# Kernel optimization log

Hardware: AMD Instinct MI355X
Metric: run time of the kernel (lower is better)

## Reference

```python
import jax, jax.numpy as jnp
import numpy as np

B, T, DIM = 2, 2048, 2048
N_HEADS, N_KV_HEADS = 16, 4
HEAD_DIM = DIM // N_HEADS  # 128
N_REP = N_HEADS // N_KV_HEADS  # 4
ROPE_THETA = 10000.0


def setup_inputs() -> dict:
    key = jax.random.key(0)
    ks = jax.random.split(key, 5)
    x = jax.random.normal(ks[0], (B, T, DIM), dtype=jnp.float32)
    # RoPE tables (equivalent to complex freqs_cis = exp(i * t * inv_freq))
    inv_freq = 1.0 / (ROPE_THETA ** (np.arange(0, HEAD_DIM, 2, dtype=np.float32) / HEAD_DIM))
    t = np.arange(T, dtype=np.float32)
    ang = np.outer(t, inv_freq)  # (T, HEAD_DIM//2)
    freqs_cos = jnp.asarray(np.cos(ang), dtype=jnp.float32)
    freqs_sin = jnp.asarray(np.sin(ang), dtype=jnp.float32)
    s = 0.02
    wq = jax.random.normal(ks[1], (DIM, N_HEADS * HEAD_DIM), dtype=jnp.float32) * s
    wk = jax.random.normal(ks[2], (DIM, N_KV_HEADS * HEAD_DIM), dtype=jnp.float32) * s
    wv = jax.random.normal(ks[3], (DIM, N_KV_HEADS * HEAD_DIM), dtype=jnp.float32) * s
    wo = jax.random.normal(ks[4], (N_HEADS * HEAD_DIM, DIM), dtype=jnp.float32) * s
    return {"x": x, "freqs_cos": freqs_cos, "freqs_sin": freqs_sin,
            "wq": wq, "wk": wk, "wv": wv, "wo": wo}


def _apply_rope(t, cos, sin):
    # t: (B, H, T, hd); cos/sin: (T, hd//2); interleaved pairs like view_as_complex
    tr = t[..., 0::2]
    ti = t[..., 1::2]
    c = cos[None, None, :, :]
    s = sin[None, None, :, :]
    out_r = tr * c - ti * s
    out_i = tr * s + ti * c
    return jnp.stack([out_r, out_i], axis=-1).reshape(t.shape)


def reference(x, freqs_cos, freqs_sin, wq, wk, wv, wo):
    Bb, Tt, C = x.shape
    q = (x @ wq).reshape(Bb, Tt, N_HEADS, HEAD_DIM).transpose(0, 2, 1, 3)      # (B,H,T,hd)
    k = (x @ wk).reshape(Bb, Tt, N_KV_HEADS, HEAD_DIM).transpose(0, 2, 1, 3)   # (B,KV,T,hd)
    v = (x @ wv).reshape(Bb, Tt, N_KV_HEADS, HEAD_DIM).transpose(0, 2, 1, 3)
    q = _apply_rope(q, freqs_cos[:Tt], freqs_sin[:Tt])
    k = _apply_rope(k, freqs_cos[:Tt], freqs_sin[:Tt])
    # GQA repeat_kv
    k = jnp.repeat(k, N_REP, axis=1)  # (B,H,T,hd)
    v = jnp.repeat(v, N_REP, axis=1)
    scale = 1.0 / jnp.sqrt(jnp.float32(HEAD_DIM))
    scores = jnp.einsum("bhqd,bhkd->bhqk", q, k) * scale
    causal = jnp.tril(jnp.ones((Tt, Tt), dtype=bool))
    scores = jnp.where(causal[None, None], scores, jnp.float32(-jnp.inf))
    attn = jax.nn.softmax(scores, axis=-1)
    out = jnp.einsum("bhqk,bhkd->bhqd", attn, v)          # (B,H,T,hd)
    out = out.transpose(0, 2, 1, 3).reshape(Bb, Tt, C)
    return out @ wo
```

## Files before the change

kernel.cpp:

```cpp
#include <hip/hip_runtime.h>
#include <hip/hip_bf16.h>

#define SEQT 2048
#define NH 16
#define HD 128

typedef __bf16 bf16;
typedef __bf16 bf16x4 __attribute__((ext_vector_type(4)));
typedef __bf16 bf16x8 __attribute__((ext_vector_type(8)));
typedef float f32x4 __attribute__((ext_vector_type(4)));
typedef float f32x16 __attribute__((ext_vector_type(16)));

__device__ inline void glds16(const bf16* g, bf16* l) {
  __builtin_amdgcn_global_load_lds(
      (const __attribute__((address_space(1))) unsigned int*)g,
      (__attribute__((address_space(3))) unsigned int*)l, 16, 0, 0);
}

__device__ inline unsigned int cvtpk(float a, float b) {
  unsigned int d;
  asm("v_cvt_pk_bf16_f32 %0, %1, %2" : "=v"(d) : "v"(a), "v"(b));
  return d;
}

__global__ __launch_bounds__(256) void k_convert(const float* __restrict__ in,
                                                 bf16* __restrict__ out, int n8) {
  int i = blockIdx.x * 256 + threadIdx.x;
  if (i >= n8) return;
  const float4* p = (const float4*)in + (size_t)i * 2;
  float4 a = p[0], b = p[1];
  bf16x8 o;
  o[0] = (bf16)a.x; o[1] = (bf16)a.y; o[2] = (bf16)a.z; o[3] = (bf16)a.w;
  o[4] = (bf16)b.x; o[5] = (bf16)b.y; o[6] = (bf16)b.z; o[7] = (bf16)b.w;
  *((bf16x8*)out + i) = o;
}

__global__ __launch_bounds__(256) void k_transpose(const float* __restrict__ in,
                                                   bf16* __restrict__ out, int R, int C) {
  __shared__ float tile[32][33];
  int c0 = blockIdx.x * 32, r0 = blockIdx.y * 32;
  int tx = threadIdx.x, ty = threadIdx.y;
#pragma unroll
  for (int i = 0; i < 4; i++)
    tile[ty + i * 8][tx] = in[(size_t)(r0 + ty + i * 8) * C + c0 + tx];
  __syncthreads();
#pragma unroll
  for (int i = 0; i < 4; i++) {
    int r = ty + i * 8;
    out[(size_t)(c0 + r) * R + r0 + tx] = (bf16)tile[tx][r];
  }
}

__global__ __launch_bounds__(256) void k_transpose3(const float* __restrict__ wq,
                                                    const float* __restrict__ wk,
                                                    const float* __restrict__ wv,
                                                    bf16* __restrict__ W) {
  __shared__ float tile[32][33];
  int bx = blockIdx.x;
  const float* src;
  bf16* dst;
  int C;
  if (bx < 64) {
    src = wq; dst = W; C = 2048;
  } else if (bx < 80) {
    src = wk; dst = W + 2048 * 2048; C = 512; bx -= 64;
  } else {
    src = wv; dst = W + 2560 * 2048; C = 512; bx -= 80;
  }
  int c0 = bx * 32, r0 = blockIdx.y * 32;
  int tx = threadIdx.x, ty = threadIdx.y;
#pragma unroll
  for (int i = 0; i < 4; i++)
    tile[ty + i * 8][tx] = src[(size_t)(r0 + ty + i * 8) * C + c0 + tx];
  __syncthreads();
#pragma unroll
  for (int i = 0; i < 4; i++) {
    int r = ty + i * 8;
    dst[(size_t)(c0 + r) * 2048 + r0 + tx] = (bf16)tile[tx][r];
  }
}

template <typename OutT>
__global__ __launch_bounds__(512, 2) void k_gemm8(const bf16* __restrict__ A,
                                                  const bf16* __restrict__ Bt,
                                                  OutT* __restrict__ C,
                                                  int nbx, int K, int ldc) {
  __shared__ bf16 AB[2][2][16384];
  int nb = gridDim.x;
  int cpx = nb >> 3;
  int bid = blockIdx.x;
  int sw = (bid & 7) * cpx + (bid >> 3);
  int bx = sw % nbx, by = sw / nbx;
  int m0 = by << 8, n0 = bx << 8;
  int tid = threadIdx.x;
  int lane = tid & 63, wid = tid >> 6;
  int wr2 = wid >> 2, wc2 = wid & 3;
  int lr = lane & 15, lg = lane >> 4;
  int lx = lr & 7;

  f32x4 acc[2][4][2][2] = {};

  int srow = tid >> 3;
  int ssl8 = ((tid & 7) ^ (srow & 7)) * 8;

#define STAGE(SBUF, SAB, SHALF, KO)                                           \
  {                                                                           \
    int ko = (KO) <= (K - 64) ? (KO) : 0;                                     \
    const bf16* gb = (SAB) ? Bt : A;                                          \
    int rb = ((SAB) ? n0 : m0) + (SHALF) * 128 + srow;                        \
    glds16(gb + (size_t)rb * K + ko + ssl8,                                   \
           &AB[SBUF][SAB][(SHALF) * 8192 + tid * 8]);                         \
    glds16(gb + (size_t)(rb + 64) * K + ko + ssl8,                            \
           &AB[SBUF][SAB][(SHALF) * 8192 + (512 + tid) * 8]);                 \
  }

#define PHASE(BUF, QM, QN, SBUF, SAB, SHALF, SKO, DOVM)                       \
  {                                                                           \
    bf16x8 af[4][2], bq[2][2];                                                \
    _Pragma("unroll") for (int mi = 0; mi < 4; mi++)                          \
      _Pragma("unroll") for (int kk = 0; kk < 2; kk++)                        \
        af[mi][kk] = *(const bf16x8*)&AB[BUF][0][                             \
            ((QM) * 128 + wr2 * 64 + mi * 16 + lr) * 64 +                     \
            (((kk * 4 + lg) ^ lx) * 8)];                                      \
    _Pragma("unroll") for (int ni = 0; ni < 2; ni++)                          \
      _Pragma("unroll") for (int kk = 0; kk < 2; kk++)                        \
        bq[ni][kk] = *(const bf16x8*)&AB[BUF][1][                             \
            ((QN) * 128 + wc2 * 32 + ni * 16 + lr) * 64 +                     \
            (((kk * 4 + lg) ^ lx) * 8)];                                      \
    STAGE(SBUF, SAB, SHALF, SKO)                                              \
    if (DOVM) { asm volatile("s_waitcnt vmcnt(4)" ::: "memory"); }            \
    __builtin_amdgcn_sched_barrier(0);                                        \
    __builtin_amdgcn_s_barrier();                                             \
    __builtin_amdgcn_sched_barrier(0);                                        \
    __builtin_amdgcn_s_setprio(1);                                            \
    _Pragma("unroll") for (int kk = 0; kk < 2; kk++)                          \
      _Pragma("unroll") for (int mi = 0; mi < 4; mi++)                        \
        _Pragma("unroll") for (int ni = 0; ni < 2; ni++)                      \
          acc[QM][mi][QN][ni] = __builtin_amdgcn_mfma_f32_16x16x32_bf16(      \
              af[mi][kk], bq[ni][kk], acc[QM][mi][QN][ni], 0, 0, 0);          \
    __builtin_amdgcn_s_setprio(0);                                            \
    __builtin_amdgcn_sched_barrier(0);                                        \
    __builtin_amdgcn_s_barrier();                                             \
    __builtin_amdgcn_sched_barrier(0);                                        \
  }

  STAGE(0, 0, 0, 0) STAGE(0, 1, 0, 0) STAGE(0, 0, 1, 0) STAGE(0, 1, 1, 0)
  STAGE(1, 0, 0, 64) STAGE(1, 1, 0, 64)
  asm volatile("s_waitcnt vmcnt(4)" ::: "memory");
  __builtin_amdgcn_sched_barrier(0);
  __builtin_amdgcn_s_barrier();
  __builtin_amdgcn_sched_barrier(0);

  int nit = K >> 7;
  for (int it = 0; it < nit; it++) {
    int kb = it << 7;
    PHASE(0, 0, 0,  1, 0, 1, kb + 64,  0)
    PHASE(0, 0, 1,  1, 1, 1, kb + 64,  0)
    PHASE(0, 1, 0,  0, 0, 0, kb + 128, 0)
    PHASE(0, 1, 1,  0, 1, 0, kb + 128, 1)
    PHASE(1, 0, 0,  0, 0, 1, kb + 128, 0)
    PHASE(1, 0, 1,  0, 1, 1, kb + 128, 0)
    PHASE(1, 1, 0,  1, 0, 0, kb + 192, 0)
    PHASE(1, 1, 1,  1, 1, 0, kb + 192, 1)
  }
#undef PHASE
#undef STAGE

  int crow = m0 + wr2 * 64 + lg * 4;
  int ccol = n0 + wc2 * 32 + lr;
#pragma unroll
  for (int qm = 0; qm < 2; qm++)
#pragma unroll
    for (int mi = 0; mi < 4; mi++)
#pragma unroll
      for (int qn = 0; qn < 2; qn++)
#pragma unroll
        for (int ni = 0; ni < 2; ni++)
#pragma unroll
          for (int r = 0; r < 4; r++)
            C[(size_t)(crow + qm * 128 + mi * 16 + r) * ldc +
              ccol + qn * 128 + ni * 16] = (OutT)acc[qm][mi][qn][ni][r];
}

template <typename OutT>
__global__ __launch_bounds__(512, 2) void k_gemm8n(const bf16* __restrict__ A,
                                                   const bf16* __restrict__ Bt,
                                                   OutT* __restrict__ C,
                                                   int nbx, int K, int ldc) {
  __shared__ bf16 Al[2][16384];
  __shared__ bf16 Bl[2][8192];
  int nb = gridDim.x;
  int cpx = nb >> 3;
  int bid = blockIdx.x;
  int sw = (bid & 7) * cpx + (bid >> 3);
  int bx = sw % nbx, by = sw / nbx;
  int m0 = by << 8, n0 = bx << 7;
  int tid = threadIdx.x;
  int lane = tid & 63, wid = tid >> 6;
  int wr2 = wid >> 2, wc2 = wid & 3;
  int lr = lane & 15, lg = lane >> 4;
  int lx = lr & 7;

  f32x4 acc[2][4][2] = {};

  int srow = tid >> 3;
  int ssl8 = ((tid & 7) ^ (srow & 7)) * 8;

#define STAGEA(SBUF, SHALF, KO)                                               \
  {                                                                           \
    int ko = (KO) <= (K - 64) ? (KO) : 0;                                     \
    int rb = m0 + (SHALF) * 128 + srow;                                       \
    glds16(A + (size_t)rb * K + ko + ssl8,                                    \
           &Al[SBUF][(SHALF) * 8192 + tid * 8]);                              \
    glds16(A + (size_t)(rb + 64) * K + ko + ssl8,                             \
           &Al[SBUF][(SHALF) * 8192 + (512 + tid) * 8]);                      \
  }
#define STAGEB(SBUF, SHALF, KO)                                               \
  {                                                                           \
    int ko = (KO) <= (K - 64) ? (KO) : 0;                                     \
    int rb = n0 + (SHALF) * 64 + srow;                                        \
    glds16(Bt + (size_t)rb * K + ko + ssl8,                                   \
           &Bl[SBUF][(SHALF) * 4096 + tid * 8]);                              \
  }

#define PHASEN(BUF, QM, QN, STG, DOVM)                                        \
  {                                                                           \
    bf16x8 af[4][2], bq[2];                                                   \
    _Pragma("unroll") for (int mi = 0; mi < 4; mi++)                          \
      _Pragma("unroll") for (int kk = 0; kk < 2; kk++)                        \
        af[mi][kk] = *(const bf16x8*)&Al[BUF][                                \
            (QM) * 8192 + (wr2 * 64 + mi * 16 + lr) * 64 +                    \
            (((kk * 4 + lg) ^ lx) * 8)];                                      \
    _Pragma("unroll") for (int kk = 0; kk < 2; kk++)                          \
      bq[kk] = *(const bf16x8*)&Bl[BUF][                                      \
          (QN) * 4096 + (wc2 * 16 + lr) * 64 + (((kk * 4 + lg) ^ lx) * 8)];   \
    STG                                                                       \
    if (DOVM) { asm volatile("s_waitcnt vmcnt(3)" ::: "memory"); }            \
    __builtin_amdgcn_sched_barrier(0);                                        \
    __builtin_amdgcn_s_barrier();                                             \
    __builtin_amdgcn_sched_barrier(0);                                        \
    __builtin_amdgcn_s_setprio(1);                                            \
    _Pragma("unroll") for (int kk = 0; kk < 2; kk++)                          \
      _Pragma("unroll") for (int mi = 0; mi < 4; mi++)                        \
        acc[QM][mi][QN] = __builtin_amdgcn_mfma_f32_16x16x32_bf16(            \
            af[mi][kk], bq[kk], acc[QM][mi][QN], 0, 0, 0);                    \
    __builtin_amdgcn_s_setprio(0);                                            \
    __builtin_amdgcn_sched_barrier(0);                                        \
    __builtin_amdgcn_s_barrier();                                             \
    __builtin_amdgcn_sched_barrier(0);                                        \
  }

  STAGEA(0, 0, 0) STAGEA(0, 1, 0) STAGEB(0, 0, 0) STAGEB(0, 1, 0)
  STAGEA(1, 0, 64) STAGEB(1, 0, 64)
  asm volatile("s_waitcnt vmcnt(3)" ::: "memory");
  __builtin_amdgcn_sched_barrier(0);
  __builtin_amdgcn_s_barrier();
  __builtin_amdgcn_sched_barrier(0);

  int nit = K >> 7;
  for (int it = 0; it < nit; it++) {
    int kb = it << 7;
    PHASEN(0, 0, 0, STAGEA(1, 1, kb + 64),  0)
    PHASEN(0, 0, 1, STAGEB(1, 1, kb + 64),  0)
    PHASEN(0, 1, 0, STAGEA(0, 0, kb + 128), 0)
    PHASEN(0, 1, 1, STAGEB(0, 0, kb + 128), 1)
    PHASEN(1, 0, 0, STAGEA(0, 1, kb + 128), 0)
    PHASEN(1, 0, 1, STAGEB(0, 1, kb + 128), 0)
    PHASEN(1, 1, 0, STAGEA(1, 0, kb + 192), 0)
    PHASEN(1, 1, 1, STAGEB(1, 0, kb + 192), 1)
  }
#undef PHASEN
#undef STAGEB
#undef STAGEA

  int crow = m0 + wr2 * 64 + lg * 4;
  int ccol = n0 + wc2 * 16 + lr;
#pragma unroll
  for (int qm = 0; qm < 2; qm++)
#pragma unroll
    for (int mi = 0; mi < 4; mi++)
#pragma unroll
      for (int qn = 0; qn < 2; qn++)
#pragma unroll
        for (int r = 0; r < 4; r++)
          C[(size_t)(crow + qm * 128 + mi * 16 + r) * ldc +
            ccol + qn * 64] = (OutT)acc[qm][mi][qn][r];
}

__global__ __launch_bounds__(256) void k_rope(bf16* __restrict__ qkv,
                                              const float* __restrict__ fcos,
                                              const float* __restrict__ fsin) {
  int gid = blockIdx.x * 256 + threadIdx.x;
  int row = gid / 160;
  int p = gid % 160;
  int head = p >> 3;
  int g8 = p & 7;
  int t = row & (SEQT - 1);
  int colbase = head < NH ? head * HD : NH * HD + (head - NH) * HD;
  bf16* ptr = qkv + (size_t)row * 3072 + colbase + g8 * 16;
  bf16x8 v0 = *(const bf16x8*)ptr;
  bf16x8 v1 = *(const bf16x8*)(ptr + 8);
  const f32x4* cp = (const f32x4*)(fcos + t * 64 + g8 * 8);
  const f32x4* sp = (const f32x4*)(fsin + t * 64 + g8 * 8);
  f32x4 c0 = cp[0], c1 = cp[1], s0 = sp[0], s1 = sp[1];
  bf16x8 o0, o1;
#pragma unroll
  for (int k = 0; k < 4; k++) {
    float a0 = (float)v0[2 * k], b0 = (float)v0[2 * k + 1];
    o0[2 * k]     = (bf16)(a0 * c0[k] - b0 * s0[k]);
    o0[2 * k + 1] = (bf16)(a0 * s0[k] + b0 * c0[k]);
    float a1 = (float)v1[2 * k], b1 = (float)v1[2 * k + 1];
    o1[2 * k]     = (bf16)(a1 * c1[k] - b1 * s1[k]);
    o1[2 * k + 1] = (bf16)(a1 * s1[k] + b1 * c1[k]);
  }
  *(bf16x8*)ptr = o0;
  *(bf16x8*)(ptr + 8) = o1;
}

__global__ __launch_bounds__(256, 2) void k_attn(const bf16* __restrict__ qkv,
                                                 bf16* __restrict__ attout) {
  __shared__ bf16 Kl[2][8192];
  __shared__ bf16 Vt[2][128][72];
  __shared__ float Tabs[4][4][32];
  int bid = blockIdx.x;
  int qt = 31 - (bid >> 5);
  int bh = bid & 31;
  int b = bh >> 4, h = bh & 15, kvh = h >> 2;
  int tid = threadIdx.x, wid = tid >> 6, lane = tid & 63;
  int kvhalf = wid >> 1, wq = wid & 1;
  int li = lane & 31, hi = lane >> 5;
  int q0 = qt * 64;
  int qmin = q0 + wq * 32, qmax = qmin + 31;
  int qlane = qmin + li;
  const float C1 = 0.12751744979927212f;

  const bf16* kgbase = qkv + (size_t)b * SEQT * 3072 + 2048 + kvh * HD;
  const bf16* vgbase = kgbase + 512;

  bf16x8 qf[8];
  {
    const bf16* qb = qkv + (size_t)(b * SEQT + qlane) * 3072 + h * HD + hi * 8;
#pragma unroll
    for (int ks = 0; ks < 8; ks++) qf[ks] = *(const bf16x8*)(qb + ks * 16);
  }

  float mrun = -INFINITY, lpart = 0.f;
  f32x16 o0 = {}, o1 = {}, o2 = {}, o3 = {};
  int nkt = qt + 1;
  int kvbase = 32 * kvhalf;

  int g = (lane >> 4) & 3;
  int lr = lane & 15;
  int kq4 = (wid * 4 + g) * 4;
  int dc = lr * 8;
  int xr = (lr & 7) << 3;
  int kvw = kq4 ^ xr;

  bf16x8 vr0, vr1, vr2, vr3;

#pragma unroll
  for (int r = 0; r < 4; r++) {
    int ci = r * 256 + tid;
    int row = ci >> 4;
    int sl = (ci & 15) ^ (row & 15);
    glds16(kgbase + (size_t)row * 3072 + sl * 8, &Kl[0][ci * 8]);
  }
  {
    const bf16* vrow = vgbase + (size_t)kq4 * 3072 + dc;
    vr0 = *(const bf16x8*)(vrow);
    vr1 = *(const bf16x8*)(vrow + 3072);
    vr2 = *(const bf16x8*)(vrow + 6144);
    vr3 = *(const bf16x8*)(vrow + 9216);
  }

  for (int kt = 0; kt < nkt; kt++) {
    int cur = kt & 1;
    int kv0 = kt * 64;
    asm volatile("s_waitcnt vmcnt(0)" ::: "memory");

#pragma unroll
    for (int j = 0; j < 8; j++) {
      bf16x4 w;
      w[0] = vr0[j]; w[1] = vr1[j]; w[2] = vr2[j]; w[3] = vr3[j];
      *(bf16x4*)&Vt[cur][dc + j][kvw] = w;
    }

    asm volatile("s_waitcnt lgkmcnt(0)" ::: "memory");
    __builtin_amdgcn_sched_barrier(0);
    __builtin_amdgcn_s_barrier();
    __builtin_amdgcn_sched_barrier(0);

    if (kt + 1 < nkt) {
      int kv1 = kv0 + 64;
      bf16* kdst = &Kl[cur ^ 1][0];
#pragma unroll
      for (int r = 0; r < 4; r++) {
        int ci = r * 256 + tid;
        int row = ci >> 4;
        int sl = (ci & 15) ^ (row & 15);
        glds16(kgbase + (size_t)(kv1 + row) * 3072 + sl * 8, kdst + ci * 8);
      }
      const bf16* vrow = vgbase + (size_t)(kv1 + kq4) * 3072 + dc;
      vr0 = *(const bf16x8*)(vrow);
      vr1 = *(const bf16x8*)(vrow + 3072);
      vr2 = *(const bf16x8*)(vrow + 6144);
      vr3 = *(const bf16x8*)(vrow + 9216);
    }

    if (kv0 + kvbase <= qmax) {
      f32x16 s0 = {};
      const char* kb0 = (const char*)&Kl[cur][0] + kvhalf * 8192 + li * 256;
      __builtin_amdgcn_s_setprio(1);
#pragma unroll
      for (int ks = 0; ks < 8; ks++) {
        int off = ((ks * 2 + hi) ^ (li & 15)) << 4;
        bf16x8 kf0 = *(const bf16x8*)(kb0 + off);
        s0 = __builtin_amdgcn_mfma_f32_32x32x16_bf16(kf0, qf[ks], s0, 0, 0, 0);
      }
      __builtin_amdgcn_s_setprio(0);

      if (kv0 + kvbase + 31 > qmin) {
        int base0 = kv0 + kvbase + 4 * hi - qlane;
#pragma unroll
        for (int r = 0; r < 16; r++) {
          int off = (r & 3) + 8 * (r >> 2);
          if (base0 + off > 0) s0[r] = -INFINITY;
        }
      }

      float pm = s0[0];
#pragma unroll
      for (int r = 1; r < 16; r++) pm = fmaxf(pm, s0[r]);
      pm = fmaxf(pm, __shfl_xor(pm, 32));

      if (!__all(pm - mrun <= 62.0f)) {
        float mnew = fmaxf(mrun, pm);
        float alpha = exp2f((mrun - mnew) * C1);
        mrun = mnew;
        lpart *= alpha;
        Tabs[0][wid][li] = alpha;
        asm volatile("s_waitcnt lgkmcnt(0)" ::: "memory");
        f32x4 a0 = *(const f32x4*)&Tabs[0][wid][4 * hi];
        f32x4 a1 = *(const f32x4*)&Tabs[0][wid][4 * hi + 8];
        f32x4 a2 = *(const f32x4*)&Tabs[0][wid][4 * hi + 16];
        f32x4 a3 = *(const f32x4*)&Tabs[0][wid][4 * hi + 24];
#define RESC_RR(rr, av)                                            \
  _Pragma("unroll") for (int i = 0; i < 4; i++) {                  \
    float f = av[i];                                               \
    o0[rr * 4 + i] *= f; o1[rr * 4 + i] *= f;                      \
    o2[rr * 4 + i] *= f; o3[rr * 4 + i] *= f;                      \
  }
        RESC_RR(0, a0) RESC_RR(1, a1) RESC_RR(2, a2) RESC_RR(3, a3)
#undef RESC_RR
      }

      float mC = mrun * C1;
      float rs = 0.f;
#pragma unroll
      for (int r = 0; r < 16; r++) {
        float p = exp2f(fmaf(s0[r], C1, -mC));
        s0[r] = p; rs += p;
      }
      lpart += rs;

      union U4 { unsigned int u[4]; bf16x8 v; };
      U4 pa0, pa1;
      {
        unsigned int e0 = cvtpk(s0[0], s0[1]), e1 = cvtpk(s0[2], s0[3]);
        unsigned int e2 = cvtpk(s0[4], s0[5]), e3 = cvtpk(s0[6], s0[7]);
        unsigned int e4 = cvtpk(s0[8], s0[9]), e5 = cvtpk(s0[10], s0[11]);
        unsigned int e6 = cvtpk(s0[12], s0[13]), e7 = cvtpk(s0[14], s0[15]);
        unsigned int t0 = __shfl_xor(e0, 32), t1 = __shfl_xor(e1, 32);
        unsigned int t2 = __shfl_xor(e2, 32), t3 = __shfl_xor(e3, 32);
        unsigned int t4 = __shfl_xor(e4, 32), t5 = __shfl_xor(e5, 32);
        unsigned int t6 = __shfl_xor(e6, 32), t7 = __shfl_xor(e7, 32);
        pa0.u[0] = hi ? t2 : e0;  pa0.u[1] = hi ? t3 : e1;
        pa0.u[2] = hi ? e2 : t0;  pa0.u[3] = hi ? e3 : t1;
        pa1.u[0] = hi ? t6 : e4;  pa1.u[1] = hi ? t7 : e5;
        pa1.u[2] = hi ? e6 : t4;  pa1.u[3] = hi ? e7 : t5;
      }

      __builtin_amdgcn_s_setprio(1);
#define PV_DB(OACC, DB)                                                      \
  {                                                                          \
    int d = DB * 32 + li;                                                    \
    int xv = ((d >> 3) & 7) << 3;                                            \
    bf16x8 vb0 = *(const bf16x8*)&Vt[cur][d][(kvbase + hi * 8) ^ xv];        \
    bf16x8 vb1 = *(const bf16x8*)&Vt[cur][d][(kvbase + 16 + hi * 8) ^ xv];   \
    OACC = __builtin_amdgcn_mfma_f32_32x32x16_bf16(pa0.v, vb0, OACC, 0, 0, 0); \
    OACC = __builtin_amdgcn_mfma_f32_32x32x16_bf16(pa1.v, vb1, OACC, 0, 0, 0); \
  }
      PV_DB(o0, 0) PV_DB(o1, 1) PV_DB(o2, 2) PV_DB(o3, 3)
#undef PV_DB
      __builtin_amdgcn_s_setprio(0);
    }
  }

  lpart += __shfl_xor(lpart, 32);
  Tabs[0][wid][li] = mrun;
  Tabs[1][wid][li] = lpart;
  asm volatile("s_waitcnt lgkmcnt(0)" ::: "memory");
  __builtin_amdgcn_s_barrier();
  int peer = wid ^ 2;
  float mP = Tabs[0][peer][li], lP = Tabs[1][peer][li];
  float mS = fmaxf(mrun, mP);
  float fMe = exp2f((mrun - mS) * C1);
  float fPe = exp2f((mP - mS) * C1);
  float lTot = lpart * fMe + lP * fPe;
  Tabs[2][wid][li] = fMe;
  Tabs[3][wid][li] = 1.f / lTot;
  asm volatile("s_waitcnt lgkmcnt(0)" ::: "memory");
  __builtin_amdgcn_s_barrier();
  f32x4 Fv0 = *(const f32x4*)&Tabs[2][wid][4 * hi];
  f32x4 Fv1 = *(const f32x4*)&Tabs[2][wid][4 * hi + 8];
  f32x4 Fv2 = *(const f32x4*)&Tabs[2][wid][4 * hi + 16];
  f32x4 Fv3 = *(const f32x4*)&Tabs[2][wid][4 * hi + 24];
  f32x4 Iv0 = *(const f32x4*)&Tabs[3][wid][4 * hi];
  f32x4 Iv1 = *(const f32x4*)&Tabs[3][wid][4 * hi + 8];
  f32x4 Iv2 = *(const f32x4*)&Tabs[3][wid][4 * hi + 16];
  f32x4 Iv3 = *(const f32x4*)&Tabs[3][wid][4 * hi + 24];

  float* X = (float*)&Kl[0][0];
  float* Xb = X + (wid & 1) * 4096;
  if (kvhalf == 1) {
#define XW_RR(OACC, DB, rr, Fv)                                              \
  _Pragma("unroll") for (int i = 0; i < 4; i++)                              \
    Xb[(4 * hi + 8 * rr + i) * 128 + DB * 32 + li] = OACC[rr * 4 + i] * Fv[i];
#define XW_DB(OACC, DB) XW_RR(OACC, DB, 0, Fv0) XW_RR(OACC, DB, 1, Fv1) \
                        XW_RR(OACC, DB, 2, Fv2) XW_RR(OACC, DB, 3, Fv3)
    XW_DB(o0, 0) XW_DB(o1, 1) XW_DB(o2, 2) XW_DB(o3, 3)
#undef XW_DB
#undef XW_RR
  }
  asm volatile("s_waitcnt lgkmcnt(0)" ::: "memory");
  __builtin_amdgcn_s_barrier();
  if (kvhalf == 0) {
#define XR_RR(OACC, DB, rr, Fv)                                              \
  _Pragma("unroll") for (int i = 0; i < 4; i++)                              \
    OACC[rr * 4 + i] = OACC[rr * 4 + i] * Fv[i] +                            \
        Xb[(4 * hi + 8 * rr + i) * 128 + DB * 32 + li];
#define XR_DB(OACC, DB) XR_RR(OACC, DB, 0, Fv0) XR_RR(OACC, DB, 1, Fv1) \
                        XR_RR(OACC, DB, 2, Fv2) XR_RR(OACC, DB, 3, Fv3)
    XR_DB(o0, 0) XR_DB(o1, 1) XR_DB(o2, 2) XR_DB(o3, 3)
#undef XR_DB
#undef XR_RR
    size_t obase = (size_t)(b * SEQT) * 2048 + h * HD;
#define STORE_RR(rr, lv)                                                     \
  _Pragma("unroll") for (int i = 0; i < 4; i++) {                            \
    int q = qmin + 4 * hi + 8 * rr + i;                                      \
    size_t rowb = obase + (size_t)q * 2048 + li;                             \
    attout[rowb + 0]  = (bf16)(o0[rr * 4 + i] * lv[i]);                      \
    attout[rowb + 32] = (bf16)(o1[rr * 4 + i] * lv[i]);                      \
    attout[rowb + 64] = (bf16)(o2[rr * 4 + i] * lv[i]);                      \
    attout[rowb + 96] = (bf16)(o3[rr * 4 + i] * lv[i]);                      \
  }
    STORE_RR(0, Iv0) STORE_RR(1, Iv1) STORE_RR(2, Iv2) STORE_RR(3, Iv3)
#undef STORE_RR
  }
}

extern "C" void kernel_launch(void* const* d_in, const int* in_sizes, int n_in,
                              void* d_out, int out_size, void* d_ws, size_t ws_size,
                              hipStream_t stream) {
  const float* x    = (const float*)d_in[0];
  const float* fcos = (const float*)d_in[1];
  const float* fsin = (const float*)d_in[2];
  const float* wq   = (const float*)d_in[3];
  const float* wk   = (const float*)d_in[4];
  const float* wv   = (const float*)d_in[5];
  const float* wo   = (const float*)d_in[6];
  float* out = (float*)d_out;

  char* ws = (char*)d_ws;
  bf16* XB  = (bf16*)ws;
  bf16* W   = (bf16*)(ws + 16777216);
  bf16* QKV = (bf16*)(ws + 16777216 + 12582912);

  dim3 tb(32, 8);
  k_transpose3<<<dim3(96, 64), tb, 0, stream>>>(wq, wk, wv, W);
  k_convert<<<4096, 256, 0, stream>>>(x, XB, 1048576);
  k_gemm8<bf16><<<192, 512, 0, stream>>>(XB, W, QKV, 12, 2048, 3072);
  k_rope<<<2560, 256, 0, stream>>>(QKV, fcos, fsin);
  k_attn<<<1024, 256, 0, stream>>>(QKV, XB);
  k_transpose<<<dim3(64, 64), tb, 0, stream>>>(wo, W, 2048, 2048);
  k_gemm8n<float><<<256, 512, 0, stream>>>(XB, W, out, 16, 2048, 2048);
}
```

Measured before the change: 220.2 us.

## Fuse RoPE into attention loads and merge wo transpose into QKV transpose

```diff
diff --git a/kernel.cpp b/kernel.cpp
--- a/kernel.cpp
+++ b/kernel.cpp
@@ -66,6 +66,39 @@
     src = wk; dst = W + 2048 * 2048; C = 512; bx -= 64;
   } else {
     src = wv; dst = W + 2560 * 2048; C = 512; bx -= 80;
+  }
+  int c0 = bx * 32, r0 = blockIdx.y * 32;
+  int tx = threadIdx.x, ty = threadIdx.y;
+#pragma unroll
+  for (int i = 0; i < 4; i++)
+    tile[ty + i * 8][tx] = src[(size_t)(r0 + ty + i * 8) * C + c0 + tx];
+  __syncthreads();
+#pragma unroll
+  for (int i = 0; i < 4; i++) {
+    int r = ty + i * 8;
+    dst[(size_t)(c0 + r) * 2048 + r0 + tx] = (bf16)tile[tx][r];
+  }
+}
+
+__global__ __launch_bounds__(256) void k_transpose4(const float* __restrict__ wq,
+                                                    const float* __restrict__ wk,
+                                                    const float* __restrict__ wv,
+                                                    const float* __restrict__ wo,
+                                                    bf16* __restrict__ W,
+                                                    bf16* __restrict__ WOT) {
+  __shared__ float tile[32][33];
+  int bx = blockIdx.x;
+  const float* src;
+  bf16* dst;
+  int C;
+  if (bx < 64) {
+    src = wq; dst = W; C = 2048;
+  } else if (bx < 80) {
+    src = wk; dst = W + 2048 * 2048; C = 512; bx -= 64;
+  } else if (bx < 96) {
+    src = wv; dst = W + 2560 * 2048; C = 512; bx -= 80;
+  } else {
+    src = wo; dst = WOT; C = 2048; bx -= 96;
   }
   int c0 = bx * 32, r0 = blockIdx.y * 32;
   int tx = threadIdx.x, ty = threadIdx.y;
@@ -287,38 +320,10 @@
             ccol + qn * 64] = (OutT)acc[qm][mi][qn][r];
 }
 
-__global__ __launch_bounds__(256) void k_rope(bf16* __restrict__ qkv,
-                                              const float* __restrict__ fcos,
-                                              const float* __restrict__ fsin) {
-  int gid = blockIdx.x * 256 + threadIdx.x;
-  int row = gid / 160;
-  int p = gid % 160;
-  int head = p >> 3;
-  int g8 = p & 7;
-  int t = row & (SEQT - 1);
-  int colbase = head < NH ? head * HD : NH * HD + (head - NH) * HD;
-  bf16* ptr = qkv + (size_t)row * 3072 + colbase + g8 * 16;
-  bf16x8 v0 = *(const bf16x8*)ptr;
-  bf16x8 v1 = *(const bf16x8*)(ptr + 8);
-  const f32x4* cp = (const f32x4*)(fcos + t * 64 + g8 * 8);
-  const f32x4* sp = (const f32x4*)(fsin + t * 64 + g8 * 8);
-  f32x4 c0 = cp[0], c1 = cp[1], s0 = sp[0], s1 = sp[1];
-  bf16x8 o0, o1;
-#pragma unroll
-  for (int k = 0; k < 4; k++) {
-    float a0 = (float)v0[2 * k], b0 = (float)v0[2 * k + 1];
-    o0[2 * k]     = (bf16)(a0 * c0[k] - b0 * s0[k]);
-    o0[2 * k + 1] = (bf16)(a0 * s0[k] + b0 * c0[k]);
-    float a1 = (float)v1[2 * k], b1 = (float)v1[2 * k + 1];
-    o1[2 * k]     = (bf16)(a1 * c1[k] - b1 * s1[k]);
-    o1[2 * k + 1] = (bf16)(a1 * s1[k] + b1 * c1[k]);
-  }
-  *(bf16x8*)ptr = o0;
-  *(bf16x8*)(ptr + 8) = o1;
-}
-
 __global__ __launch_bounds__(256, 2) void k_attn(const bf16* __restrict__ qkv,
-                                                 bf16* __restrict__ attout) {
+                                                 bf16* __restrict__ attout,
+                                                 const float* __restrict__ fcos,
+                                                 const float* __restrict__ fsin) {
   __shared__ bf16 Kl[2][8192];
   __shared__ bf16 Vt[2][128][72];
   __shared__ float Tabs[4][4][32];
@@ -340,14 +345,30 @@
   bf16x8 qf[8];
   {
     const bf16* qb = qkv + (size_t)(b * SEQT + qlane) * 3072 + h * HD + hi * 8;
-#pragma unroll
-    for (int ks = 0; ks < 8; ks++) qf[ks] = *(const bf16x8*)(qb + ks * 16);
+    const float* cb = fcos + qlane * 64 + hi * 4;
+    const float* sb = fsin + qlane * 64 + hi * 4;
+#pragma unroll
+    for (int ks = 0; ks < 8; ks++) {
+      bf16x8 v = *(const bf16x8*)(qb + ks * 16);
+      f32x4 c = *(const f32x4*)(cb + ks * 8);
+      f32x4 s = *(const f32x4*)(sb + ks * 8);
+#pragma unroll
+      for (int j = 0; j < 4; j++) {
+        float a = (float)v[2 * j], bb = (float)v[2 * j + 1];
+        qf[ks][2 * j]     = (bf16)(a * c[j] - bb * s[j]);
+        qf[ks][2 * j + 1] = (bf16)(a * s[j] + bb * c[j]);
+      }
+    }
   }
 
   float mrun = -INFINITY, lpart = 0.f;
   f32x16 o0 = {}, o1 = {}, o2 = {}, o3 = {};
   int nkt = qt + 1;
   int kvbase = 32 * kvhalf;
+
+  int kslot = tid & 15;
+  int krow0 = tid >> 4;
+  int kphys8 = ((kslot ^ krow0) & 15) * 8;
 
   int g = (lane >> 4) & 3;
   int lr = lane & 15;
@@ -356,14 +377,16 @@
   int xr = (lr & 7) << 3;
   int kvw = kq4 ^ xr;
 
+  bf16x8 krg[4];
+  f32x4 ck[4], sk[4];
   bf16x8 vr0, vr1, vr2, vr3;
 
 #pragma unroll
   for (int r = 0; r < 4; r++) {
-    int ci = r * 256 + tid;
-    int row = ci >> 4;
-    int sl = (ci & 15) ^ (row & 15);
-    glds16(kgbase + (size_t)row * 3072 + sl * 8, &Kl[0][ci * 8]);
+    int row = r * 16 + krow0;
+    krg[r] = *(const bf16x8*)(kgbase + (size_t)row * 3072 + kslot * 8);
+    ck[r] = *(const f32x4*)(fcos + (size_t)row * 64 + kslot * 4);
+    sk[r] = *(const f32x4*)(fsin + (size_t)row * 64 + kslot * 4);
   }
   {
     const bf16* vrow = vgbase + (size_t)kq4 * 3072 + dc;
@@ -379,6 +402,18 @@
     asm volatile("s_waitcnt vmcnt(0)" ::: "memory");
 
 #pragma unroll
+    for (int r = 0; r < 4; r++) {
+      bf16x8 kw;
+#pragma unroll
+      for (int j = 0; j < 4; j++) {
+        float a = (float)krg[r][2 * j], bb = (float)krg[r][2 * j + 1];
+        kw[2 * j]     = (bf16)(a * ck[r][j] - bb * sk[r][j]);
+        kw[2 * j + 1] = (bf16)(a * sk[r][j] + bb * ck[r][j]);
+      }
+      *(bf16x8*)&Kl[cur][(r * 16 + krow0) * 128 + kphys8] = kw;
+    }
+
+#pragma unroll
     for (int j = 0; j < 8; j++) {
       bf16x4 w;
       w[0] = vr0[j]; w[1] = vr1[j]; w[2] = vr2[j]; w[3] = vr3[j];
@@ -392,13 +427,12 @@
 
     if (kt + 1 < nkt) {
       int kv1 = kv0 + 64;
-      bf16* kdst = &Kl[cur ^ 1][0];
 #pragma unroll
       for (int r = 0; r < 4; r++) {
-        int ci = r * 256 + tid;
-        int row = ci >> 4;
-        int sl = (ci & 15) ^ (row & 15);
-        glds16(kgbase + (size_t)(kv1 + row) * 3072 + sl * 8, kdst + ci * 8);
+        int row = kv1 + r * 16 + krow0;
+        krg[r] = *(const bf16x8*)(kgbase + (size_t)row * 3072 + kslot * 8);
+        ck[r] = *(const f32x4*)(fcos + (size_t)row * 64 + kslot * 4);
+        sk[r] = *(const f32x4*)(fsin + (size_t)row * 64 + kslot * 4);
       }
       const bf16* vrow = vgbase + (size_t)(kv1 + kq4) * 3072 + dc;
       vr0 = *(const bf16x8*)(vrow);
@@ -575,13 +609,20 @@
   bf16* XB  = (bf16*)ws;
   bf16* W   = (bf16*)(ws + 16777216);
   bf16* QKV = (bf16*)(ws + 16777216 + 12582912);
+  bool bigws = ws_size >= 62914560ull;
+  bf16* WOT = bigws ? (bf16*)(ws + 54525952) : W;
 
   dim3 tb(32, 8);
-  k_transpose3<<<dim3(96, 64), tb, 0, stream>>>(wq, wk, wv, W);
+  if (bigws) {
+    k_transpose4<<<dim3(160, 64), tb, 0, stream>>>(wq, wk, wv, wo, W, WOT);
+  } else {
+    k_transpose3<<<dim3(96, 64), tb, 0, stream>>>(wq, wk, wv, W);
+  }
   k_convert<<<4096, 256, 0, stream>>>(x, XB, 1048576);
   k_gemm8<bf16><<<192, 512, 0, stream>>>(XB, W, QKV, 12, 2048, 3072);
-  k_rope<<<2560, 256, 0, stream>>>(QKV, fcos, fsin);
-  k_attn<<<1024, 256, 0, stream>>>(QKV, XB);
-  k_transpose<<<dim3(64, 64), tb, 0, stream>>>(wo, W, 2048, 2048);
-  k_gemm8n<float><<<256, 512, 0, stream>>>(XB, W, out, 16, 2048, 2048);
-}
+  k_attn<<<1024, 256, 0, stream>>>(QKV, XB, fcos, fsin);
+  if (!bigws) {
+    k_transpose<<<dim3(64, 64), tb, 0, stream>>>(wo, W, 2048, 2048);
+  }
+  k_gemm8n<float><<<256, 512, 0, stream>>>(XB, WOT, out, 16, 2048, 2048);
+}
```

After: 237.2 us. 7.7% more time.
